# Optimization experiments

Measured on AMD Instinct MI355X. Metric: run time of the kernel, lower is better.

## Reference

```python
import jax, jax.numpy as jnp
import numpy as np

N, F, E = 1024, 32, 20


def setup_inputs() -> dict:
    key = jax.random.key(0)
    ks = jax.random.split(key, 18)
    f32 = jnp.float32
    nrm = lambda k, shape, s=1.0: (jax.random.normal(k, shape, f32) * s)
    scalar = nrm(ks[0], (N, 1, F))
    vector = nrm(ks[1], (N, 3, F))
    expansion = nrm(ks[2], (N, N, E))
    d = nrm(ks[3], (N, N, 3))
    direction = d / (jnp.linalg.norm(d, axis=-1, keepdims=True) + 1e-6)
    mask = (jax.random.uniform(ks[4], (N, N, 1)) < 0.9).astype(f32)
    w = 0.1  # weight scale
    return {
        "scalar": scalar, "vector": vector, "expansion": expansion,
        "direction": direction, "mask": mask,
        # message.msg_left: Linear(F,F) -> SiLU -> Linear(F,3F)
        "mL_w1": nrm(ks[5], (F, F), w), "mL_b1": jnp.zeros((F,), f32),
        "mL_w2": nrm(ks[6], (F, 3 * F), w), "mL_b2": jnp.zeros((3 * F,), f32),
        # message.msg_right: Linear(E, 3F)
        "mR_w": nrm(ks[7], (E, 3 * F), w), "mR_b": jnp.zeros((3 * F,), f32),
        # update.upd_right: Linear(2F,F) -> SiLU -> Linear(F,3F)
        "uR_w1": nrm(ks[8], (2 * F, F), w), "uR_b1": jnp.zeros((F,), f32),
        "uR_w2": nrm(ks[9], (F, 3 * F), w), "uR_b2": jnp.zeros((3 * F,), f32),
        # update.U / update.V: Linear(F,F,bias=False)
        "U_w": nrm(ks[10], (F, F), w),
        "V_w": nrm(ks[11], (F, F), w),
    }


def _message(s, v, expansion, direction, mask,
             mL_w1, mL_b1, mL_w2, mL_b2, mR_w, mR_b):
    # msg_left(s): [N,1,F] -> [N,1,3F]
    left = jax.nn.silu(s @ mL_w1 + mL_b1) @ mL_w2 + mL_b2
    # msg_right(expansion): [N,N,E] -> [N,N,3F] -> [N,N,1,3F]
    right = (expansion @ mR_w + mR_b)[..., None, :]
    prod = left * right                      # [N,N,1,3F]
    a, b, c = jnp.split(prod, 3, axis=-1)    # each [N,N,1,F]
    mask_ = mask[..., None]                  # [N,N,1,1]
    delta_s = jnp.sum(mask_ * b, axis=-3)    # [N,1,F]
    dv = v * a + direction[..., None] * c    # [N,N,3,F]
    delta_v = jnp.sum(mask_ * dv, axis=-3)   # [N,3,F]
    return delta_s, delta_v


def _update(scalar, vector, uR_w1, uR_b1, uR_w2, uR_b2, U_w, V_w):
    left = vector @ U_w                      # [N,3,F]
    right = vector @ V_w                     # [N,3,F]
    right_norm = jnp.linalg.norm(right, axis=-2, keepdims=True)   # [N,1,F]
    feats = jnp.concatenate((scalar, right_norm), axis=-1)        # [N,1,2F]
    feats = jax.nn.silu(feats @ uR_w1 + uR_b1) @ uR_w2 + uR_b2    # [N,1,3F]
    a, b, c = jnp.split(feats, 3, axis=-1)
    delta_v = a * left                                            # [N,3,F]
    inner = jnp.sum(left * right, axis=-2, keepdims=True)         # [N,1,F]
    delta_s = inner * b + c
    return delta_s, delta_v


def reference(scalar, vector, expansion, direction, mask,
              mL_w1, mL_b1, mL_w2, mL_b2, mR_w, mR_b,
              uR_w1, uR_b1, uR_w2, uR_b2, U_w, V_w):
    ds, dv = _message(scalar, vector, expansion, direction, mask,
                      mL_w1, mL_b1, mL_w2, mL_b2, mR_w, mR_b)
    scalar = scalar + ds
    vector = vector + dv
    ds, dv = _update(scalar, vector, uR_w1, uR_b1, uR_w2, uR_b2, U_w, V_w)
    return scalar + ds, vector + dv
```

## Files before the change

kernel.cpp:

```cpp
#include <hip/hip_runtime.h>
#include <hip/hip_bf16.h>
#include <math.h>

#define NN 1024
#define JS 256
#define NSL 4
#define PB 72
#define LP 40
#define WBUF 5376

typedef __attribute__((ext_vector_type(8))) short v8s;
typedef __attribute__((ext_vector_type(4))) float v4f;

#define MFMA(a, b, c) __builtin_amdgcn_mfma_f32_16x16x32_bf16((a), (b), (c), 0, 0, 0)

static __device__ __forceinline__ float silu_f(float x) {
    return x / (1.0f + __expf(-x));
}
static __device__ __forceinline__ unsigned short f2bf(float x) {
    __hip_bfloat16 h = __float2bfloat16(x);
    unsigned short u; __builtin_memcpy(&u, &h, 2); return u;
}
static __device__ __forceinline__ unsigned pack2bf(float lo, float hi) {
    __hip_bfloat162 h = __float22bfloat162_rn(make_float2(lo, hi));
    unsigned u; __builtin_memcpy(&u, &h, 4); return u;
}

extern "C" __global__ __launch_bounds__(128)
void node_kernel(const float* __restrict__ scalar,
                 const float* __restrict__ vector,
                 const float* __restrict__ mL_w1, const float* __restrict__ mL_b1,
                 const float* __restrict__ mL_w2, const float* __restrict__ mL_b2,
                 unsigned short* __restrict__ RT)
{
    const int j = blockIdx.x;
    const int t = threadIdx.x;
    __shared__ float ss[32], sh[32], sleft[96];

    if (t < 32) ss[t] = scalar[j * 32 + t];
    __syncthreads();
    if (t < 32) {
        float a = mL_b1[t];
        #pragma unroll
        for (int k = 0; k < 32; k++) a = fmaf(ss[k], mL_w1[k * 32 + t], a);
        sh[t] = silu_f(a);
    }
    __syncthreads();
    if (t < 96) {
        float a = mL_b2[t];
        #pragma unroll
        for (int k = 0; k < 32; k++) a = fmaf(sh[k], mL_w2[k * 96 + t], a);
        sleft[t] = a;
    }
    __syncthreads();
    for (int n = t; n < 160; n += 128) {
        float val;
        if (n < 32)        val = sleft[32 + n];
        else if (n < 128)  val = vector[j * 96 + (n - 32)] * sleft[(n - 32) & 31];
        else               val = sleft[64 + (n - 128)];
        RT[(size_t)n * NN + j] = f2bf(val);
    }
}

extern "C" __global__ __launch_bounds__(256, 3)
void edge_mfma_kernel(const float* __restrict__ expansion,
                      const float* __restrict__ direction,
                      const float* __restrict__ mask,
                      const float* __restrict__ mR_w, const float* __restrict__ mR_b,
                      const unsigned short* __restrict__ RT,
                      float* __restrict__ part)
{
    const int t = threadIdx.x;
    const int wave = t >> 6;
    const int lane = t & 63;
    const int lrow = lane & 15;
    const int quad = lane >> 4;
    const int jp = lane >> 2;
    const int g  = lane & 3;
    const int jl = jp * 2;

    const int bx = blockIdx.x;
    const int slice = bx & (NSL - 1);
    const int j0 = slice * JS;
    const int i = (bx >> 2) * 2 + (wave >> 1);

    __shared__ __align__(16) unsigned short BSm[160 * PB];
    __shared__ __align__(16) char Wm[4 * WBUF];

    for (int u = t; u < 160 * 8; u += 256) {
        const int row = u >> 3, seg = u & 7;
        *(uint4*)(BSm + row * PB + seg * 8) =
            *(const uint4*)(RT + (size_t)row * NN + j0 + seg * 8);
    }
    __syncthreads();

    char* wbase = Wm + wave * WBUF;

    if ((wave & 1) == 0) {
        unsigned short* L1 = (unsigned short*)wbase;
        float* S = (float*)wbase;

        v4f acc[16];
        #pragma unroll
        for (int q = 0; q < 16; ++q) acc[q] = (v4f){0.f, 0.f, 0.f, 0.f};

        float4 fa, fb, ca, cb; float m0, m1;
        {
            const size_t jg = (size_t)i * NN + j0 + jl;
            fa = *(const float4*)(expansion + jg * 20 + 4 * g);
            fb = *(const float4*)(expansion + (jg + 1) * 20 + 4 * g);
            ca = *(const float4*)(expansion + jg * 20 + 16);
            cb = *(const float4*)(expansion + (jg + 1) * 20 + 16);
            m0 = mask[jg]; m1 = mask[jg + 1];
        }

        for (int ss2 = 0; ss2 < 4; ++ss2) {
            #pragma unroll
            for (int ch = 0; ch < 2; ++ch) {
                {
                    const float ea[4] = {fa.x, fa.y, fa.z, fa.w};
                    const float eb[4] = {fb.x, fb.y, fb.z, fb.w};
                    #pragma unroll
                    for (int k = 0; k < 4; ++k)
                        *(unsigned*)(L1 + (4 * g + k) * LP + jl) =
                            pack2bf(m0 * ea[k], m1 * eb[k]);
                    if (g == 3) {
                        const float caa[4] = {ca.x, ca.y, ca.z, ca.w};
                        const float cbb[4] = {cb.x, cb.y, cb.z, cb.w};
                        #pragma unroll
                        for (int k = 0; k < 4; ++k)
                            *(unsigned*)(L1 + (16 + k) * LP + jl) =
                                pack2bf(m0 * caa[k], m1 * cbb[k]);
                    }
                    if (g == 0) *(unsigned*)(L1 + 20 * LP + jl) = pack2bf(m0, m1);
                }
                {
                    const int u = ss2 * 2 + ch;
                    const int un = (u < 7) ? u + 1 : 7;
                    const size_t jg = (size_t)i * NN + j0 + un * 32 + jl;
                    fa = *(const float4*)(expansion + jg * 20 + 4 * g);
                    fb = *(const float4*)(expansion + (jg + 1) * 20 + 4 * g);
                    ca = *(const float4*)(expansion + jg * 20 + 16);
                    cb = *(const float4*)(expansion + (jg + 1) * 20 + 16);
                    m0 = mask[jg]; m1 = mask[jg + 1];
                }
                {
                    const int ko = quad * 8;
                    const int kl = ch * 32 + ko;
                    const v8s a0 = *(const v8s*)(L1 + lrow * LP + ko);
                    const v8s a1 = *(const v8s*)(L1 + (16 + lrow) * LP + ko);
                    #pragma unroll
                    for (int nt = 0; nt < 8; ++nt) {
                        const v8s b = *(const v8s*)(BSm + (nt * 16 + lrow) * PB + kl);
                        acc[nt]     = MFMA(a0, b, acc[nt]);
                        acc[8 + nt] = MFMA(a1, b, acc[8 + nt]);
                    }
                }
            }
            __syncthreads();
            if (ss2 < 3) {
                for (int u2 = t; u2 < 160 * 8; u2 += 256) {
                    const int row = u2 >> 3, seg = u2 & 7;
                    *(uint4*)(BSm + row * PB + seg * 8) =
                        *(const uint4*)(RT + (size_t)row * NN + j0 + (ss2 + 1) * 64 + seg * 8);
                }
                __syncthreads();
            }
        }

        float* pdst = part + ((size_t)i * NSL + slice) * 224;
        #pragma unroll
        for (int h = 0; h < 2; ++h) {
            #pragma unroll
            for (int mt = 0; mt < 2; ++mt)
            #pragma unroll
            for (int q = 0; q < 4; ++q)
            #pragma unroll
            for (int r = 0; r < 4; ++r) {
                const int row = mt * 16 + quad * 4 + r;
                if (row <= 20) S[row * 64 + q * 16 + lrow] = acc[mt * 8 + h * 4 + q][r];
            }
            const int col = h * 64 + lane;
            const int fw = (col < 32) ? (32 + col) : ((col - 32) & 31);
            float v = mR_b[fw] * S[20 * 64 + lane];
            #pragma unroll
            for (int e = 0; e < 20; ++e)
                v = fmaf(mR_w[e * 96 + fw], S[e * 64 + lane], v);
            pdst[col] = v;
        }
    } else {
        unsigned short* L2 = (unsigned short*)wbase;
        float* S = (float*)wbase;

        v4f acc[8];
        #pragma unroll
        for (int q = 0; q < 8; ++q) acc[q] = (v4f){0.f, 0.f, 0.f, 0.f};

        float4 fa, fb, ca, cb;
        float m0, m1, da0, da1, da2, db0, db1, db2;
        {
            const size_t jg = (size_t)i * NN + j0 + jl;
            fa = *(const float4*)(expansion + jg * 20 + 4 * g);
            fb = *(const float4*)(expansion + (jg + 1) * 20 + 4 * g);
            ca = *(const float4*)(expansion + jg * 20 + 16);
            cb = *(const float4*)(expansion + (jg + 1) * 20 + 16);
            m0 = mask[jg]; m1 = mask[jg + 1];
            da0 = direction[jg * 3 + 0]; da1 = direction[jg * 3 + 1]; da2 = direction[jg * 3 + 2];
            db0 = direction[(jg + 1) * 3 + 0]; db1 = direction[(jg + 1) * 3 + 1]; db2 = direction[(jg + 1) * 3 + 2];
        }

        for (int ss2 = 0; ss2 < 4; ++ss2) {
            #pragma unroll
            for (int ch = 0; ch < 2; ++ch) {
                {
                    const float pa[3] = {m0 * da0, m0 * da1, m0 * da2};
                    const float pb[3] = {m1 * db0, m1 * db1, m1 * db2};
                    const float ea[4] = {fa.x, fa.y, fa.z, fa.w};
                    const float eb[4] = {fb.x, fb.y, fb.z, fb.w};
                    #pragma unroll
                    for (int d = 0; d < 3; ++d)
                        #pragma unroll
                        for (int k = 0; k < 4; ++k)
                            *(unsigned*)(L2 + (d * 20 + 4 * g + k) * LP + jl) =
                                pack2bf(pa[d] * ea[k], pb[d] * eb[k]);
                    if (g < 3) {
                        const float sa = (g == 0) ? pa[0] : ((g == 1) ? pa[1] : pa[2]);
                        const float sb = (g == 0) ? pb[0] : ((g == 1) ? pb[1] : pb[2]);
                        const float caa[4] = {ca.x, ca.y, ca.z, ca.w};
                        const float cbb[4] = {cb.x, cb.y, cb.z, cb.w};
                        #pragma unroll
                        for (int k = 0; k < 4; ++k)
                            *(unsigned*)(L2 + (g * 20 + 16 + k) * LP + jl) =
                                pack2bf(sa * caa[k], sb * cbb[k]);
                    } else {
                        *(unsigned*)(L2 + (60 + 0) * LP + jl) = pack2bf(pa[0], pb[0]);
                        *(unsigned*)(L2 + (60 + 1) * LP + jl) = pack2bf(pa[1], pb[1]);
                        *(unsigned*)(L2 + (60 + 2) * LP + jl) = pack2bf(pa[2], pb[2]);
                    }
                }
                {
                    const int u = ss2 * 2 + ch;
                    const int un = (u < 7) ? u + 1 : 7;
                    const size_t jg = (size_t)i * NN + j0 + un * 32 + jl;
                    fa = *(const float4*)(expansion + jg * 20 + 4 * g);
                    fb = *(const float4*)(expansion + (jg + 1) * 20 + 4 * g);
                    ca = *(const float4*)(expansion + jg * 20 + 16);
                    cb = *(const float4*)(expansion + (jg + 1) * 20 + 16);
                    m0 = mask[jg]; m1 = mask[jg + 1];
                    da0 = direction[jg * 3 + 0]; da1 = direction[jg * 3 + 1]; da2 = direction[jg * 3 + 2];
                    db0 = direction[(jg + 1) * 3 + 0]; db1 = direction[(jg + 1) * 3 + 1]; db2 = direction[(jg + 1) * 3 + 2];
                }
                {
                    const int ko = quad * 8;
                    const int kl = ch * 32 + ko;
                    const v8s c0 = *(const v8s*)(L2 + (lrow) * LP + ko);
                    const v8s c1 = *(const v8s*)(L2 + (16 + lrow) * LP + ko);
                    const v8s c2 = *(const v8s*)(L2 + (32 + lrow) * LP + ko);
                    const v8s c3 = *(const v8s*)(L2 + (48 + lrow) * LP + ko);
                    const v8s b0 = *(const v8s*)(BSm + (128 + lrow) * PB + kl);
                    const v8s b1 = *(const v8s*)(BSm + (144 + lrow) * PB + kl);
                    acc[0] = MFMA(c0, b0, acc[0]); acc[1] = MFMA(c0, b1, acc[1]);
                    acc[2] = MFMA(c1, b0, acc[2]); acc[3] = MFMA(c1, b1, acc[3]);
                    acc[4] = MFMA(c2, b0, acc[4]); acc[5] = MFMA(c2, b1, acc[5]);
                    acc[6] = MFMA(c3, b0, acc[6]); acc[7] = MFMA(c3, b1, acc[7]);
                }
            }
            __syncthreads();
            if (ss2 < 3) {
                for (int u2 = t; u2 < 160 * 8; u2 += 256) {
                    const int row = u2 >> 3, seg = u2 & 7;
                    *(uint4*)(BSm + row * PB + seg * 8) =
                        *(const uint4*)(RT + (size_t)row * NN + j0 + (ss2 + 1) * 64 + seg * 8);
                }
                __syncthreads();
            }
        }

        float* pdst = part + ((size_t)i * NSL + slice) * 224;
        #pragma unroll
        for (int h2 = 0; h2 < 2; ++h2) {
            #pragma unroll
            for (int mt = 0; mt < 4; ++mt)
            #pragma unroll
            for (int r = 0; r < 4; ++r) {
                const int row = mt * 16 + quad * 4 + r;
                if (row <= 62) S[row * 16 + lrow] = acc[mt * 2 + h2][r];
            }
            if (lane < 48) {
                const int dd = lane >> 4, f16 = lane & 15;
                const int f = h2 * 16 + f16;
                float v = mR_b[64 + f] * S[(60 + dd) * 16 + f16];
                #pragma unroll
                for (int e = 0; e < 20; ++e)
                    v = fmaf(mR_w[e * 96 + 64 + f], S[(dd * 20 + e) * 16 + f16], v);
                pdst[128 + dd * 32 + f] = v;
            }
        }
    }
}

extern "C" __global__ __launch_bounds__(256)
void combine_kernel(const float* __restrict__ scalar,
                    const float* __restrict__ vector,
                    const float* __restrict__ uR_w1, const float* __restrict__ uR_b1,
                    const float* __restrict__ uR_w2, const float* __restrict__ uR_b2,
                    const float* __restrict__ U_w,  const float* __restrict__ V_w,
                    const float* __restrict__ part,
                    float* __restrict__ out)
{
    const int i = blockIdx.x;
    const int t = threadIdx.x;
    __shared__ float pcomb[224];
    __shared__ float snew[32], vnew[96];
    __shared__ float lU[96], rV[96], rnorm[32], h2[32], f2[96];

    if (t < 224) {
        const float* p = part + (size_t)i * NSL * 224 + t;
        float a = 0.f;
        #pragma unroll
        for (int s = 0; s < NSL; ++s) a += p[s * 224];
        pcomb[t] = a;
    }
    __syncthreads();

    if (t < 128) {
        const int d = t >> 5, ff = t & 31;
        if (d == 0) snew[ff] = scalar[i * 32 + ff] + pcomb[ff];
        else {
            const int q = t - 32;
            vnew[q] = vector[i * 96 + q] + pcomb[32 + q] + pcomb[128 + q];
        }
    }
    __syncthreads();

    if (t < 96) {
        const int d = t >> 5, ff = t & 31;
        float a = 0.0f;
        #pragma unroll
        for (int k = 0; k < 32; k++) a = fmaf(vnew[d * 32 + k], U_w[k * 32 + ff], a);
        lU[t] = a;
    } else if (t >= 128 && t < 224) {
        const int dt = t - 128, d = dt >> 5, ff = dt & 31;
        float a = 0.0f;
        #pragma unroll
        for (int k = 0; k < 32; k++) a = fmaf(vnew[d * 32 + k], V_w[k * 32 + ff], a);
        rV[dt] = a;
    }
    __syncthreads();
    if (t < 32) {
        const float a = rV[t] * rV[t] + rV[32 + t] * rV[32 + t] + rV[64 + t] * rV[64 + t];
        rnorm[t] = sqrtf(a);
    }
    __syncthreads();
    if (t < 32) {
        float a = uR_b1[t];
        #pragma unroll
        for (int k = 0; k < 32; k++) a = fmaf(snew[k],  uR_w1[k * 32 + t], a);
        #pragma unroll
        for (int k = 0; k < 32; k++) a = fmaf(rnorm[k], uR_w1[(32 + k) * 32 + t], a);
        h2[t] = silu_f(a);
    }
    __syncthreads();
    if (t < 96) {
        float a = uR_b2[t];
        #pragma unroll
        for (int k = 0; k < 32; k++) a = fmaf(h2[k], uR_w2[k * 96 + t], a);
        f2[t] = a;
    }
    __syncthreads();
    if (t < 32) {
        const float inner = lU[t] * rV[t] + lU[32 + t] * rV[32 + t] + lU[64 + t] * rV[64 + t];
        out[i * 32 + t] = snew[t] + inner * f2[32 + t] + f2[64 + t];
    } else if (t >= 64 && t < 160) {
        const int dt = t - 64, ff = dt & 31;
        out[32768 + i * 96 + dt] = vnew[dt] + f2[ff] * lU[dt];
    }
}

extern "C" void kernel_launch(void* const* d_in, const int* in_sizes, int n_in,
                              void* d_out, int out_size, void* d_ws, size_t ws_size,
                              hipStream_t stream) {
    const float* scalar    = (const float*)d_in[0];
    const float* vector    = (const float*)d_in[1];
    const float* expansion = (const float*)d_in[2];
    const float* direction = (const float*)d_in[3];
    const float* mask      = (const float*)d_in[4];
    const float* mL_w1     = (const float*)d_in[5];
    const float* mL_b1     = (const float*)d_in[6];
    const float* mL_w2     = (const float*)d_in[7];
    const float* mL_b2     = (const float*)d_in[8];
    const float* mR_w      = (const float*)d_in[9];
    const float* mR_b      = (const float*)d_in[10];
    const float* uR_w1     = (const float*)d_in[11];
    const float* uR_b1     = (const float*)d_in[12];
    const float* uR_w2     = (const float*)d_in[13];
    const float* uR_b2     = (const float*)d_in[14];
    const float* U_w       = (const float*)d_in[15];
    const float* V_w       = (const float*)d_in[16];
    float* out = (float*)d_out;

    unsigned short* RT = (unsigned short*)d_ws;
    float* part = (float*)((char*)d_ws + 160 * NN * 2);

    hipLaunchKernelGGL(node_kernel, dim3(NN), dim3(128), 0, stream,
                       scalar, vector, mL_w1, mL_b1, mL_w2, mL_b2, RT);
    hipLaunchKernelGGL(edge_mfma_kernel, dim3(2048), dim3(256), 0, stream,
                       expansion, direction, mask, mR_w, mR_b, RT, part);
    hipLaunchKernelGGL(combine_kernel, dim3(NN), dim3(256), 0, stream,
                       scalar, vector, uR_w1, uR_b1, uR_w2, uR_b2, U_w, V_w,
                       part, out);
}
```

Measured before the change: 206.1 us.

## Load MFMA B operands directly from global memory, dropping the shared staging buffer

Removes the block-wide shared-memory staging of the RT (transposed right weights) tile, along with its __syncthreads barriers. Each wave now loads its B fragments for the MFMAs straight from global/L2 into registers at the start of each 32-wide chunk. This eliminates block-level synchronisation and LDS traffic, and lets the waves run independently. In exchange every wave issues redundant global loads of the same RT data, which adds register pressure and L2 load latency on the critical path before the MFMAs.

New measurement: 223.9 us. +8.6%, slower.

```diff
diff --git a/kernel.cpp b/kernel.cpp
--- a/kernel.cpp
+++ b/kernel.cpp
@@ -5,7 +5,6 @@
 #define NN 1024
 #define JS 256
 #define NSL 4
-#define PB 72
 #define LP 40
 #define WBUF 5376
 
@@ -84,16 +83,7 @@
     const int j0 = slice * JS;
     const int i = (bx >> 2) * 2 + (wave >> 1);
 
-    __shared__ __align__(16) unsigned short BSm[160 * PB];
     __shared__ __align__(16) char Wm[4 * WBUF];
-
-    for (int u = t; u < 160 * 8; u += 256) {
-        const int row = u >> 3, seg = u & 7;
-        *(uint4*)(BSm + row * PB + seg * 8) =
-            *(const uint4*)(RT + (size_t)row * NN + j0 + seg * 8);
-    }
-    __syncthreads();
-
     char* wbase = Wm + wave * WBUF;
 
     if ((wave & 1) == 0) {
@@ -114,57 +104,49 @@
             m0 = mask[jg]; m1 = mask[jg + 1];
         }
 
-        for (int ss2 = 0; ss2 < 4; ++ss2) {
-            #pragma unroll
-            for (int ch = 0; ch < 2; ++ch) {
-                {
-                    const float ea[4] = {fa.x, fa.y, fa.z, fa.w};
-                    const float eb[4] = {fb.x, fb.y, fb.z, fb.w};
+        const int ko = quad * 8;
+        for (int u = 0; u < 8; ++u) {
+            v8s b[8];
+            {
+                const unsigned short* Bg = RT + (size_t)lrow * NN + j0 + u * 32 + ko;
+                #pragma unroll
+                for (int nt = 0; nt < 8; ++nt)
+                    b[nt] = *(const v8s*)(Bg + (size_t)nt * 16 * NN);
+            }
+            {
+                const float ea[4] = {fa.x, fa.y, fa.z, fa.w};
+                const float eb[4] = {fb.x, fb.y, fb.z, fb.w};
+                #pragma unroll
+                for (int k = 0; k < 4; ++k)
+                    *(unsigned*)(L1 + (4 * g + k) * LP + jl) =
+                        pack2bf(m0 * ea[k], m1 * eb[k]);
+                if (g == 3) {
+                    const float caa[4] = {ca.x, ca.y, ca.z, ca.w};
+                    const float cbb[4] = {cb.x, cb.y, cb.z, cb.w};
                     #pragma unroll
                     for (int k = 0; k < 4; ++k)
-                        *(unsigned*)(L1 + (4 * g + k) * LP + jl) =
-                            pack2bf(m0 * ea[k], m1 * eb[k]);
-                    if (g == 3) {
-                        const float caa[4] = {ca.x, ca.y, ca.z, ca.w};
-                        const float cbb[4] = {cb.x, cb.y, cb.z, cb.w};
-                        #pragma unroll
-                        for (int k = 0; k < 4; ++k)
-                            *(unsigned*)(L1 + (16 + k) * LP + jl) =
-                                pack2bf(m0 * caa[k], m1 * cbb[k]);
-                    }
-                    if (g == 0) *(unsigned*)(L1 + 20 * LP + jl) = pack2bf(m0, m1);
+                        *(unsigned*)(L1 + (16 + k) * LP + jl) =
+                            pack2bf(m0 * caa[k], m1 * cbb[k]);
                 }
-                {
-                    const int u = ss2 * 2 + ch;
-                    const int un = (u < 7) ? u + 1 : 7;
-                    const size_t jg = (size_t)i * NN + j0 + un * 32 + jl;
-                    fa = *(const float4*)(expansion + jg * 20 + 4 * g);
-                    fb = *(const float4*)(expansion + (jg + 1) * 20 + 4 * g);
-                    ca = *(const float4*)(expansion + jg * 20 + 16);
-                    cb = *(const float4*)(expansion + (jg + 1) * 20 + 16);
-                    m0 = mask[jg]; m1 = mask[jg + 1];
+                if (g == 0) *(unsigned*)(L1 + 20 * LP + jl) = pack2bf(m0, m1);
+            }
+            {
+                const int un = (u < 7) ? u + 1 : 7;
+                const size_t jg = (size_t)i * NN + j0 + un * 32 + jl;
+                fa = *(const float4*)(expansion + jg * 20 + 4 * g);
+                fb = *(const float4*)(expansion + (jg + 1) * 20 + 4 * g);
+                ca = *(const float4*)(expansion + jg * 20 + 16);
+                cb = *(const float4*)(expansion + (jg + 1) * 20 + 16);
+                m0 = mask[jg]; m1 = mask[jg + 1];
+            }
+            {
+                const v8s a0 = *(const v8s*)(L1 + lrow * LP + ko);
+                const v8s a1 = *(const v8s*)(L1 + (16 + lrow) * LP + ko);
+                #pragma unroll
+                for (int nt = 0; nt < 8; ++nt) {
+                    acc[nt]     = MFMA(a0, b[nt], acc[nt]);
+                    acc[8 + nt] = MFMA(a1, b[nt], acc[8 + nt]);
                 }
-                {
-                    const int ko = quad * 8;
-                    const int kl = ch * 32 + ko;
-                    const v8s a0 = *(const v8s*)(L1 + lrow * LP + ko);
-                    const v8s a1 = *(const v8s*)(L1 + (16 + lrow) * LP + ko);
-                    #pragma unroll
-                    for (int nt = 0; nt < 8; ++nt) {
-                        const v8s b = *(const v8s*)(BSm + (nt * 16 + lrow) * PB + kl);
-                        acc[nt]     = MFMA(a0, b, acc[nt]);
-                        acc[8 + nt] = MFMA(a1, b, acc[8 + nt]);
-                    }
-                }
-            }
-            __syncthreads();
-            if (ss2 < 3) {
-                for (int u2 = t; u2 < 160 * 8; u2 += 256) {
-                    const int row = u2 >> 3, seg = u2 & 7;
-                    *(uint4*)(BSm + row * PB + seg * 8) =
-                        *(const uint4*)(RT + (size_t)row * NN + j0 + (ss2 + 1) * 64 + seg * 8);
-                }
-                __syncthreads();
             }
         }
 
@@ -209,70 +191,60 @@
             db0 = direction[(jg + 1) * 3 + 0]; db1 = direction[(jg + 1) * 3 + 1]; db2 = direction[(jg + 1) * 3 + 2];
         }
 
-        for (int ss2 = 0; ss2 < 4; ++ss2) {
-            #pragma unroll
-            for (int ch = 0; ch < 2; ++ch) {
-                {
-                    const float pa[3] = {m0 * da0, m0 * da1, m0 * da2};
-                    const float pb[3] = {m1 * db0, m1 * db1, m1 * db2};
-                    const float ea[4] = {fa.x, fa.y, fa.z, fa.w};
-                    const float eb[4] = {fb.x, fb.y, fb.z, fb.w};
+        const int ko = quad * 8;
+        for (int u = 0; u < 8; ++u) {
+            v8s b0, b1;
+            {
+                const unsigned short* Bg = RT + (size_t)(128 + lrow) * NN + j0 + u * 32 + ko;
+                b0 = *(const v8s*)(Bg);
+                b1 = *(const v8s*)(Bg + 16 * NN);
+            }
+            {
+                const float pa[3] = {m0 * da0, m0 * da1, m0 * da2};
+                const float pb[3] = {m1 * db0, m1 * db1, m1 * db2};
+                const float ea[4] = {fa.x, fa.y, fa.z, fa.w};
+                const float eb[4] = {fb.x, fb.y, fb.z, fb.w};
+                #pragma unroll
+                for (int d = 0; d < 3; ++d)
                     #pragma unroll
-                    for (int d = 0; d < 3; ++d)
-                        #pragma unroll
-                        for (int k = 0; k < 4; ++k)
-                            *(unsigned*)(L2 + (d * 20 + 4 * g + k) * LP + jl) =
-                                pack2bf(pa[d] * ea[k], pb[d] * eb[k]);
-                    if (g < 3) {
-                        const float sa = (g == 0) ? pa[0] : ((g == 1) ? pa[1] : pa[2]);
-                        const float sb = (g == 0) ? pb[0] : ((g == 1) ? pb[1] : pb[2]);
-                        const float caa[4] = {ca.x, ca.y, ca.z, ca.w};
-                        const float cbb[4] = {cb.x, cb.y, cb.z, cb.w};
-                        #pragma unroll
-                        for (int k = 0; k < 4; ++k)
-                            *(unsigned*)(L2 + (g * 20 + 16 + k) * LP + jl) =
-                                pack2bf(sa * caa[k], sb * cbb[k]);
-                    } else {
-                        *(unsigned*)(L2 + (60 + 0) * LP + jl) = pack2bf(pa[0], pb[0]);
-                        *(unsigned*)(L2 + (60 + 1) * LP + jl) = pack2bf(pa[1], pb[1]);
-                        *(unsigned*)(L2 + (60 + 2) * LP + jl) = pack2bf(pa[2], pb[2]);
-                    }
+                    for (int k = 0; k < 4; ++k)
+                        *(unsigned*)(L2 + (d * 20 + 4 * g + k) * LP + jl) =
+                            pack2bf(pa[d] * ea[k], pb[d] * eb[k]);
+                if (g < 3) {
+                    const float sa = (g == 0) ? pa[0] : ((g == 1) ? pa[1] : pa[2]);
+                    const float sb = (g == 0) ? pb[0] : ((g == 1) ? pb[1] : pb[2]);
+                    const float caa[4] = {ca.x, ca.y, ca.z, ca.w};
+                    const float cbb[4] = {cb.x, cb.y, cb.z, cb.w};
+                    #pragma unroll
+                    for (int k = 0; k < 4; ++k)
+                        *(unsigned*)(L2 + (g * 20 + 16 + k) * LP + jl) =
+                            pack2bf(sa * caa[k], sb * cbb[k]);
+                } else {
+                    *(unsigned*)(L2 + (60 + 0) * LP + jl) = pack2bf(pa[0], pb[0]);
+                    *(unsigned*)(L2 + (60 + 1) * LP + jl) = pack2bf(pa[1], pb[1]);
+                    *(unsigned*)(L2 + (60 + 2) * LP + jl) = pack2bf(pa[2], pb[2]);
                 }
-                {
-                    const int u = ss2 * 2 + ch;
-                    const int un = (u < 7) ? u + 1 : 7;
-                    const size_t jg = (size_t)i * NN + j0 + un * 32 + jl;
-                    fa = *(const float4*)(expansion + jg * 20 + 4 * g);
-                    fb = *(const float4*)(expansion + (jg + 1) * 20 + 4 * g);
-                    ca = *(const float4*)(expansion + jg * 20 + 16);
-                    cb = *(const float4*)(expansion + (jg + 1) * 20 + 16);
-                    m0 = mask[jg]; m1 = mask[jg + 1];
-                    da0 = direction[jg * 3 + 0]; da1 = direction[jg * 3 + 1]; da2 = direction[jg * 3 + 2];
-                    db0 = direction[(jg + 1) * 3 + 0]; db1 = direction[(jg + 1) * 3 + 1]; db2 = direction[(jg + 1) * 3 + 2];
-                }
-                {
-                    const int ko = quad * 8;
-                    const int kl = ch * 32 + ko;
-                    const v8s c0 = *(const v8s*)(L2 + (lrow) * LP + ko);
-                    const v8s c1 = *(const v8s*)(L2 + (16 + lrow) * LP + ko);
-                    const v8s c2 = *(const v8s*)(L2 + (32 + lrow) * LP + ko);
-                    const v8s c3 = *(const v8s*)(L2 + (48 + lrow) * LP + ko);
-                    const v8s b0 = *(const v8s*)(BSm + (128 + lrow) * PB + kl);
-                    const v8s b1 = *(const v8s*)(BSm + (144 + lrow) * PB + kl);
-                    acc[0] = MFMA(c0, b0, acc[0]); acc[1] = MFMA(c0, b1, acc[1]);
-                    acc[2] = MFMA(c1, b0, acc[2]); acc[3] = MFMA(c1, b1, acc[3]);
-                    acc[4] = MFMA(c2, b0, acc[4]); acc[5] = MFMA(c2, b1, acc[5]);
-                    acc[6] = MFMA(c3, b0, acc[6]); acc[7] = MFMA(c3, b1, acc[7]);
-                }
-            }
-            __syncthreads();
-            if (ss2 < 3) {
-                for (int u2 = t; u2 < 160 * 8; u2 += 256) {
-                    const int row = u2 >> 3, seg = u2 & 7;
-                    *(uint4*)(BSm + row * PB + seg * 8) =
-                        *(const uint4*)(RT + (size_t)row * NN + j0 + (ss2 + 1) * 64 + seg * 8);
-                }
-                __syncthreads();
+            }
+            {
+                const int un = (u < 7) ? u + 1 : 7;
+                const size_t jg = (size_t)i * NN + j0 + un * 32 + jl;
+                fa = *(const float4*)(expansion + jg * 20 + 4 * g);
+                fb = *(const float4*)(expansion + (jg + 1) * 20 + 4 * g);
+                ca = *(const float4*)(expansion + jg * 20 + 16);
+                cb = *(const float4*)(expansion + (jg + 1) * 20 + 16);
+                m0 = mask[jg]; m1 = mask[jg + 1];
+                da0 = direction[jg * 3 + 0]; da1 = direction[jg * 3 + 1]; da2 = direction[jg * 3 + 2];
+                db0 = direction[(jg + 1) * 3 + 0]; db1 = direction[(jg + 1) * 3 + 1]; db2 = direction[(jg + 1) * 3 + 2];
+            }
+            {
+                const v8s c0 = *(const v8s*)(L2 + (lrow) * LP + ko);
+                const v8s c1 = *(const v8s*)(L2 + (16 + lrow) * LP + ko);
+                const v8s c2 = *(const v8s*)(L2 + (32 + lrow) * LP + ko);
+                const v8s c3 = *(const v8s*)(L2 + (48 + lrow) * LP + ko);
+                acc[0] = MFMA(c0, b0, acc[0]); acc[1] = MFMA(c0, b1, acc[1]);
+                acc[2] = MFMA(c1, b0, acc[2]); acc[3] = MFMA(c1, b1, acc[3]);
+                acc[4] = MFMA(c2, b0, acc[4]); acc[5] = MFMA(c2, b1, acc[5]);
+                acc[6] = MFMA(c3, b0, acc[6]); acc[7] = MFMA(c3, b1, acc[7]);
             }
         }
 
```

## Prefetch next RT tile into registers and shrink LDS to raise occupancy

Applied to the files above, without the earlier changes.

The next 64-column slice of the RT bf16 table is now loaded from global memory into registers at the start of each outer iteration, so the loads overlap the MFMA work. The registers are written to shared memory after the barrier. The per-wave scratch area is split: staging buffers stay in a smaller Wm region, and the epilogue reduction buffers reuse BSm once the MFMA loop is done. This lowers LDS use, and launch bounds are raised from 3 to 4 blocks per CU. Barriers become a custom lgkmcnt wait plus s_barrier. The added prefetch registers may pressure the register budget at higher occupancy, and aliasing S onto BSm relies on all waves having finished reading BSm before the epilogue.

Result: slower. 229.6 us (+11.4%).

```diff
diff --git a/kernel.cpp b/kernel.cpp
--- a/kernel.cpp
+++ b/kernel.cpp
@@ -7,12 +7,13 @@
 #define NSL 4
 #define PB 72
 #define LP 40
-#define WBUF 5376
 
 typedef __attribute__((ext_vector_type(8))) short v8s;
 typedef __attribute__((ext_vector_type(4))) float v4f;
 
 #define MFMA(a, b, c) __builtin_amdgcn_mfma_f32_16x16x32_bf16((a), (b), (c), 0, 0, 0)
+
+#define BAR() asm volatile("s_waitcnt lgkmcnt(0)\n\ts_barrier" ::: "memory")
 
 static __device__ __forceinline__ float silu_f(float x) {
     return x / (1.0f + __expf(-x));
@@ -62,7 +63,7 @@
     }
 }
 
-extern "C" __global__ __launch_bounds__(256, 3)
+extern "C" __global__ __launch_bounds__(256, 4)
 void edge_mfma_kernel(const float* __restrict__ expansion,
                       const float* __restrict__ direction,
                       const float* __restrict__ mask,
@@ -85,20 +86,26 @@
     const int i = (bx >> 2) * 2 + (wave >> 1);
 
     __shared__ __align__(16) unsigned short BSm[160 * PB];
-    __shared__ __align__(16) char Wm[4 * WBUF];
-
-    for (int u = t; u < 160 * 8; u += 256) {
-        const int row = u >> 3, seg = u & 7;
-        *(uint4*)(BSm + row * PB + seg * 8) =
-            *(const uint4*)(RT + (size_t)row * NN + j0 + seg * 8);
-    }
-    __syncthreads();
-
-    char* wbase = Wm + wave * WBUF;
+    __shared__ __align__(16) char Wm[13824];
+
+    {
+        uint4 st[5];
+        #pragma unroll
+        for (int k = 0; k < 5; ++k) {
+            const int u = t + k * 256, row = u >> 3, seg = u & 7;
+            st[k] = *(const uint4*)(RT + (size_t)row * NN + j0 + seg * 8);
+        }
+        #pragma unroll
+        for (int k = 0; k < 5; ++k) {
+            const int u = t + k * 256, row = u >> 3, seg = u & 7;
+            *(uint4*)(BSm + row * PB + seg * 8) = st[k];
+        }
+    }
+    BAR();
 
     if ((wave & 1) == 0) {
-        unsigned short* L1 = (unsigned short*)wbase;
-        float* S = (float*)wbase;
+        unsigned short* L1 = (unsigned short*)(Wm + (wave >> 1) * 6912);
+        float* S = (float*)((char*)BSm + (wave >> 1) * 5376);
 
         v4f acc[16];
         #pragma unroll
@@ -115,6 +122,14 @@
         }
 
         for (int ss2 = 0; ss2 < 4; ++ss2) {
+            uint4 st[5];
+            if (ss2 < 3) {
+                #pragma unroll
+                for (int k = 0; k < 5; ++k) {
+                    const int u = t + k * 256, row = u >> 3, seg = u & 7;
+                    st[k] = *(const uint4*)(RT + (size_t)row * NN + j0 + (ss2 + 1) * 64 + seg * 8);
+                }
+            }
             #pragma unroll
             for (int ch = 0; ch < 2; ++ch) {
                 {
@@ -157,14 +172,14 @@
                     }
                 }
             }
-            __syncthreads();
+            BAR();
             if (ss2 < 3) {
-                for (int u2 = t; u2 < 160 * 8; u2 += 256) {
-                    const int row = u2 >> 3, seg = u2 & 7;
-                    *(uint4*)(BSm + row * PB + seg * 8) =
-                        *(const uint4*)(RT + (size_t)row * NN + j0 + (ss2 + 1) * 64 + seg * 8);
-                }
-                __syncthreads();
+                #pragma unroll
+                for (int k = 0; k < 5; ++k) {
+                    const int u = t + k * 256, row = u >> 3, seg = u & 7;
+                    *(uint4*)(BSm + row * PB + seg * 8) = st[k];
+                }
+                BAR();
             }
         }
 
@@ -189,8 +204,8 @@
             pdst[col] = v;
         }
     } else {
-        unsigned short* L2 = (unsigned short*)wbase;
-        float* S = (float*)wbase;
+        unsigned short* L2 = (unsigned short*)(Wm + 1792 + (wave >> 1) * 6912);
+        float* S = (float*)((char*)BSm + 10752 + (wave >> 1) * 4032);
 
         v4f acc[8];
         #pragma unroll
@@ -210,6 +225,14 @@
         }
 
         for (int ss2 = 0; ss2 < 4; ++ss2) {
+            uint4 st[5];
+            if (ss2 < 3) {
+                #pragma unroll
+                for (int k = 0; k < 5; ++k) {
+                    const int u = t + k * 256, row = u >> 3, seg = u & 7;
+                    st[k] = *(const uint4*)(RT + (size_t)row * NN + j0 + (ss2 + 1) * 64 + seg * 8);
+                }
+            }
             #pragma unroll
             for (int ch = 0; ch < 2; ++ch) {
                 {
@@ -265,14 +288,14 @@
                     acc[6] = MFMA(c3, b0, acc[6]); acc[7] = MFMA(c3, b1, acc[7]);
                 }
             }
-            __syncthreads();
+            BAR();
             if (ss2 < 3) {
-                for (int u2 = t; u2 < 160 * 8; u2 += 256) {
-                    const int row = u2 >> 3, seg = u2 & 7;
-                    *(uint4*)(BSm + row * PB + seg * 8) =
-                        *(const uint4*)(RT + (size_t)row * NN + j0 + (ss2 + 1) * 64 + seg * 8);
-                }
-                __syncthreads();
+                #pragma unroll
+                for (int k = 0; k < 5; ++k) {
+                    const int u = t + k * 256, row = u >> 3, seg = u & 7;
+                    *(uint4*)(BSm + row * PB + seg * 8) = st[k];
+                }
+                BAR();
             }
         }
 
```
